# Optimization experiments

Measured on AMD Instinct MI355X. Metric: run time of the kernel, lower is better.

## Reference

```python
import jax, jax.numpy as jnp
import numpy as np

GRID_SIZE = 30
HIDDEN = 16

def _rbf_kan_layer(x, base_weight, spline_weight, grid):
    # x: [N, in], base_weight: [out, in], spline_weight: [in*G, out]
    base = x @ base_weight.T                                   # [N, out]
    basis = jnp.exp(-20.0 * (x[..., None] - grid) ** 2)        # [N, in, G]
    basis = basis.reshape(x.shape[0], -1)                      # [N, in*G]
    return base + basis @ spline_weight


def setup_inputs() -> dict:
    key = jax.random.key(0)
    ks = jax.random.split(key, 6)
    T = 100000
    t = (jnp.arange(T, dtype=jnp.float32) / T).reshape(T, 1)   # time grid in [0,1), dt = 1/T
    I_init = jax.random.uniform(ks[0], (1,), dtype=jnp.float32) * 0.1
    spline_weight1 = jax.random.normal(ks[1], (1 * GRID_SIZE, HIDDEN), dtype=jnp.float32) * 0.1
    base_weight1 = jax.random.normal(ks[2], (HIDDEN, 1), dtype=jnp.float32) * 0.1
    spline_weight2 = jax.random.normal(ks[3], (HIDDEN * GRID_SIZE, 1), dtype=jnp.float32) * 0.1
    base_weight2 = jax.random.normal(ks[4], (1, HIDDEN), dtype=jnp.float32) * 0.1
    gamma_param = jnp.array([2.0], dtype=jnp.float32)
    return {"t": t, "I_init": I_init,
            "spline_weight1": spline_weight1, "base_weight1": base_weight1,
            "spline_weight2": spline_weight2, "base_weight2": base_weight2,
            "gamma_param": gamma_param}


def reference(t, I_init, spline_weight1, base_weight1, spline_weight2, base_weight2, gamma_param):
    grid = jnp.linspace(0.0, 1.0, GRID_SIZE).astype(t.dtype)
    h = _rbf_kan_layer(t, base_weight1, spline_weight1, grid)      # [T, 16]
    out = _rbf_kan_layer(h, base_weight2, spline_weight2, grid)    # [T, 1]
    betas = jax.nn.softplus(out)                                   # [T, 1]
    gamma = jax.nn.softplus(gamma_param)                           # [1]
    dt = t[1, 0] - t[0, 0]

    I0 = I_init                                                    # [1]
    S0 = 1.0 - I0                                                  # [1]

    def step(carry, beta):
        S, I = carry
        dI = beta * S * I - gamma * I
        S_new = jnp.clip(S - beta * S * I * dt, 0.0, 1.0)
        I_new = jnp.clip(I + dI * dt, 0.0, 1.0)
        return (S_new, I_new), I_new

    _, sim_I = jax.lax.scan(step, (S0, I0), betas)                 # sim_I: [T, 1]
    return sim_I
```

## Files before the change

kernel.cpp:

```cpp
#include <hip/hip_runtime.h>
#include <hip/hip_bf16.h>

#define KAN_GRID 30
#define KAN_HID  16

#define PK   2500
#define PL   40
#define SNPT 10
#define CBLK ((PK + 255) / 256)

__global__ __launch_bounds__(256) void kan_betas_kernel(
    const float* __restrict__ t,
    const float* __restrict__ sw1,
    const float* __restrict__ bw1,
    const float* __restrict__ sw2,
    const float* __restrict__ bw2,
    float* __restrict__ beta_dt,
    int* __restrict__ bar,
    int T, int K, int L)
{
    __shared__ float s_sw1[KAN_GRID * KAN_HID];
    __shared__ float s_sw2[KAN_HID * KAN_GRID];
    __shared__ float s_bw1[KAN_HID];
    __shared__ float s_bw2[KAN_HID];

    if (bar && blockIdx.x == 0 && threadIdx.x < 2) bar[threadIdx.x] = 0;

    for (int i = threadIdx.x; i < KAN_GRID * KAN_HID; i += blockDim.x) {
        s_sw1[i] = sw1[i];
        s_sw2[i] = sw2[i];
    }
    if (threadIdx.x < KAN_HID) {
        s_bw1[threadIdx.x] = bw1[threadIdx.x];
        s_bw2[threadIdx.x] = bw2[threadIdx.x];
    }
    __syncthreads();

    int m = blockIdx.x * blockDim.x + threadIdx.x;
    if (m >= T) return;

    int n = (m % K) * L + m / K;

    float tv = t[n];
    float dt = t[1] - t[0];

    float h[KAN_HID];
#pragma unroll
    for (int j = 0; j < KAN_HID; ++j) h[j] = tv * s_bw1[j];

#pragma unroll
    for (int g = 0; g < KAN_GRID; ++g) {
        float d = tv - (float)g * (1.0f / 29.0f);
        float e = __expf(-20.0f * d * d);
#pragma unroll
        for (int j = 0; j < KAN_HID; ++j)
            h[j] = fmaf(e, s_sw1[g * KAN_HID + j], h[j]);
    }

    float out = 0.0f;
#pragma unroll
    for (int j = 0; j < KAN_HID; ++j) out = fmaf(h[j], s_bw2[j], out);

#pragma unroll
    for (int j = 0; j < KAN_HID; ++j) {
        float hv = h[j];
#pragma unroll
        for (int g = 0; g < KAN_GRID; ++g) {
            float d = hv - (float)g * (1.0f / 29.0f);
            out = fmaf(__expf(-20.0f * d * d), s_sw2[j * KAN_GRID + g], out);
        }
    }

    float beta = fmaxf(out, 0.0f) + log1pf(__expf(-fabsf(out)));
    beta_dt[m] = beta * dt;
}

#define STEP_O(BDT, DST)                            \
    {                                               \
        float x  = S * I;                           \
        float q  = fmaf(-gdt, I, I);                \
        float Sn = fmaf(-(BDT), x, S);              \
        float In = fmaf((BDT), x, q);               \
        Sn = fminf(fmaxf(Sn, 0.0f), 1.0f);          \
        In = fminf(fmaxf(In, 0.0f), 1.0f);          \
        S = Sn; I = In; (DST) = In;                 \
    }

#define STEP_J(BDT)                                          \
    {                                                        \
        float x  = S * I;                                    \
        float u  = (BDT) * I;                                \
        float v  = (BDT) * S;                                \
        float q  = fmaf(-gdt, I, I);                         \
        float Sn = fmaf(-(BDT), x, S);                       \
        float In = fmaf((BDT), x, q);                        \
        Sn = fminf(fmaxf(Sn, 0.0f), 1.0f);                   \
        In = fminf(fmaxf(In, 0.0f), 1.0f);                   \
        float w  = g1 + v;                                   \
        float a2 = fmaf(-v, jc, fmaf(-u, ja, ja));           \
        float b2 = fmaf(-v, jd, fmaf(-u, jb, jb));           \
        float c2 = fmaf(w, jc, u * ja);                      \
        float d2 = fmaf(w, jd, u * jb);                      \
        S = Sn; I = In; ja = a2; jb = b2; jc = c2; jd = d2;  \
    }

#define SOFTPLUS(X) (fmaxf((X), 0.0f) + log1pf(__expf(-fabsf(X))))

#define COMPOSE(ra,rb,rc,rd,rs,ri, La,Lb,Lc,Ld,Ls,Li, Ea,Eb,Ec,Ed,Es,Ei)   \
    {                                                                      \
        ra = fmaf(La, Ea, Lb * Ec);                                        \
        rb = fmaf(La, Eb, Lb * Ed);                                        \
        rc = fmaf(Lc, Ea, Ld * Ec);                                        \
        rd = fmaf(Lc, Eb, Ld * Ed);                                        \
        rs = fmaf(La, Es, fmaf(Lb, Ei, Ls));                               \
        ri = fmaf(Lc, Es, fmaf(Ld, Ei, Li));                               \
    }

__device__ __forceinline__ void grid_barrier(int* bar, int nblk) {
    __syncthreads();
    __threadfence();
    if (threadIdx.x == 0) {
        __hip_atomic_fetch_add(bar, 1, __ATOMIC_RELEASE,
                               __HIP_MEMORY_SCOPE_AGENT);
        while (__hip_atomic_load(bar, __ATOMIC_RELAXED,
                                 __HIP_MEMORY_SCOPE_AGENT) < nblk)
            __builtin_amdgcn_s_sleep(1);
    }
    __syncthreads();
    __threadfence();
}

__device__ __forceinline__ void block_affine_scan(
    const float* __restrict__ ja, const float* __restrict__ jb,
    const float* __restrict__ jc, const float* __restrict__ jd,
    const float* __restrict__ cs, const float* __restrict__ ci,
    int K, float S0, float I0,
    float2* g_lds, float (*wm)[6], float (*we)[6])
{
    int tid  = threadIdx.x;
    int lane = tid & 63;
    int wid  = tid >> 6;

    float Fa[SNPT], Fb[SNPT], Fc[SNPT], Fd[SNPT], Fs[SNPT], Fi[SNPT];
    float ma = 1.0f, mb = 0.0f, mc = 0.0f, md = 1.0f, ms = 0.0f, mi = 0.0f;
#pragma unroll
    for (int i = 0; i < SNPT; ++i) {
        int e = tid * SNPT + i;
        if (e < K) {
            Fa[i] = ja[e]; Fb[i] = jb[e]; Fc[i] = jc[e];
            Fd[i] = jd[e]; Fs[i] = cs[e]; Fi[i] = ci[e];
        } else {
            Fa[i] = 1.0f; Fb[i] = 0.0f; Fc[i] = 0.0f;
            Fd[i] = 1.0f; Fs[i] = 0.0f; Fi[i] = 0.0f;
        }
        float na, nb, nc, nd, ns, ni;
        COMPOSE(na,nb,nc,nd,ns,ni, Fa[i],Fb[i],Fc[i],Fd[i],Fs[i],Fi[i],
                                   ma,mb,mc,md,ms,mi);
        ma=na; mb=nb; mc=nc; md=nd; ms=ns; mi=ni;
    }

    for (int off = 1; off < 64; off <<= 1) {
        float pa = __shfl_up(ma, off), pb = __shfl_up(mb, off);
        float pc = __shfl_up(mc, off), pd = __shfl_up(md, off);
        float ps = __shfl_up(ms, off), pi = __shfl_up(mi, off);
        if (lane >= off) {
            float na, nb, nc, nd, ns, ni;
            COMPOSE(na,nb,nc,nd,ns,ni, ma,mb,mc,md,ms,mi, pa,pb,pc,pd,ps,pi);
            ma=na; mb=nb; mc=nc; md=nd; ms=ns; mi=ni;
        }
    }

    if (lane == 63) {
        wm[wid][0]=ma; wm[wid][1]=mb; wm[wid][2]=mc;
        wm[wid][3]=md; wm[wid][4]=ms; wm[wid][5]=mi;
    }
    __syncthreads();

    if (tid == 0) {
        float ra=1.0f, rb=0.0f, rc=0.0f, rd=1.0f, rs=0.0f, ri=0.0f;
        for (int w = 0; w < 4; ++w) {
            we[w][0]=ra; we[w][1]=rb; we[w][2]=rc;
            we[w][3]=rd; we[w][4]=rs; we[w][5]=ri;
            float na, nb, nc, nd, ns, ni;
            COMPOSE(na,nb,nc,nd,ns,ni,
                    wm[w][0],wm[w][1],wm[w][2],wm[w][3],wm[w][4],wm[w][5],
                    ra,rb,rc,rd,rs,ri);
            ra=na; rb=nb; rc=nc; rd=nd; rs=ns; ri=ni;
        }
    }
    __syncthreads();

    float xa = __shfl_up(ma, 1), xb = __shfl_up(mb, 1);
    float xc = __shfl_up(mc, 1), xd = __shfl_up(md, 1);
    float xs = __shfl_up(ms, 1), xi = __shfl_up(mi, 1);
    if (lane == 0) { xa=1.0f; xb=0.0f; xc=0.0f; xd=1.0f; xs=0.0f; xi=0.0f; }
    float Ca, Cb, Cc, Cd, Cs, Ci;
    COMPOSE(Ca,Cb,Cc,Cd,Cs,Ci, xa,xb,xc,xd,xs,xi,
            we[wid][0],we[wid][1],we[wid][2],we[wid][3],we[wid][4],we[wid][5]);

#pragma unroll
    for (int i = 0; i < SNPT; ++i) {
        int e = tid * SNPT + i;
        if (e < K) {
            float gS = fmaf(Ca, S0, fmaf(Cb, I0, Cs));
            float gI = fmaf(Cc, S0, fmaf(Cd, I0, Ci));
            g_lds[e] = make_float2(gS, gI);
        }
        float na, nb, nc, nd, ns, ni;
        COMPOSE(na,nb,nc,nd,ns,ni, Fa[i],Fb[i],Fc[i],Fd[i],Fs[i],Fi[i],
                                   Ca,Cb,Cc,Cd,Cs,Ci);
        Ca=na; Cb=nb; Cc=nc; Cd=nd; Cs=ns; Ci=ni;
    }
    __syncthreads();
}

template<int L>
__global__ __launch_bounds__(256, 1) void sir_fused_kernel(
    const float* __restrict__ t,
    const float* __restrict__ I_init,
    const float* __restrict__ gamma_param,
    const float* __restrict__ beta_t,
    float* __restrict__ A,
    float* __restrict__ B,
    int* __restrict__ bar,
    float* __restrict__ out,
    int K)
{
    __shared__ float2 g_lds[PK];
    __shared__ float wm[4][6], we[4][6];

    float dt = t[1] - t[0];
    float gdt = SOFTPLUS(gamma_param[0]) * dt;
    float g1 = 1.0f - gdt;
    float I0 = I_init[0];
    float S0 = 1.0f - I0;

    int k = blockIdx.x * blockDim.x + threadIdx.x;

    float b[L];
    if (k < K) {
#pragma unroll
        for (int s = 0; s < L; ++s) b[s] = beta_t[s * K + k];
    }

    if (k < K) {
        float S = S0, I = I0;
        float ja = 1.0f, jb = 0.0f, jc = 0.0f, jd = 1.0f;
#pragma unroll
        for (int s = 0; s < L; ++s) { float bdt = b[s]; STEP_J(bdt); }
        A[k]       = ja; A[K + k]   = jb; A[2*K + k] = jc; A[3*K + k] = jd;
        A[4*K + k] = S - fmaf(ja, S0, jb * I0);
        A[5*K + k] = I - fmaf(jc, S0, jd * I0);
    }
    grid_barrier(bar, gridDim.x);

    block_affine_scan(A, A + K, A + 2*K, A + 3*K, A + 4*K, A + 5*K,
                      K, S0, I0, g_lds, wm, we);
    if (k < K) {
        float2 g = g_lds[k];
        float S = g.x, I = g.y;
        float ja = 1.0f, jb = 0.0f, jc = 0.0f, jd = 1.0f;
#pragma unroll
        for (int s = 0; s < L; ++s) { float bdt = b[s]; STEP_J(bdt); }
        B[k]       = ja; B[K + k]   = jb; B[2*K + k] = jc; B[3*K + k] = jd;
        B[4*K + k] = S - fmaf(ja, g.x, jb * g.y);
        B[5*K + k] = I - fmaf(jc, g.x, jd * g.y);
    }
    grid_barrier(bar + 1, gridDim.x);

    block_affine_scan(B, B + K, B + 2*K, B + 3*K, B + 4*K, B + 5*K,
                      K, S0, I0, g_lds, wm, we);
    if (k < K) {
        float2 g = g_lds[k];
        float S = g.x, I = g.y;
        float4* o4 = (float4*)(out + (size_t)k * L);
#pragma unroll
        for (int i = 0; i < L / 4; ++i) {
            float4 r;
            STEP_O(b[4*i],     r.x);
            STEP_O(b[4*i + 1], r.y);
            STEP_O(b[4*i + 2], r.z);
            STEP_O(b[4*i + 3], r.w);
            o4[i] = r;
        }
    }
}

__global__ void kan_sir_scan_kernel(
    const float* __restrict__ t,
    const float* __restrict__ I_init,
    const float* __restrict__ gamma_param,
    const float* beta_dt,
    float* out,
    int T)
{
    if (threadIdx.x != 0 || blockIdx.x != 0) return;

    float dt = t[1] - t[0];
    float gdt = SOFTPLUS(gamma_param[0]) * dt;

    float I = I_init[0];
    float S = 1.0f - I;

    const float4* b4 = (const float4*)beta_dt;
    float4* o4 = (float4*)out;
    int nvec = T >> 2;

    const int PF = 8;
    float4 buf[PF];
#pragma unroll
    for (int i = 0; i < PF; ++i)
        buf[i] = (i < nvec) ? b4[i] : float4{0.0f, 0.0f, 0.0f, 0.0f};

    for (int base = 0; base < nvec; base += PF) {
#pragma unroll
        for (int i = 0; i < PF; ++i) {
            int c = base + i;
            if (c >= nvec) break;
            float4 b = buf[i];
            int nxt = c + PF;
            if (nxt < nvec) buf[i] = b4[nxt];

            float4 r;
            STEP_O(b.x, r.x);
            STEP_O(b.y, r.y);
            STEP_O(b.z, r.z);
            STEP_O(b.w, r.w);
            o4[c] = r;
        }
    }
    for (int n = nvec << 2; n < T; ++n) {
        float bdt = beta_dt[n];
        float r;
        STEP_O(bdt, r);
        out[n] = r;
    }
}

extern "C" void kernel_launch(void* const* d_in, const int* in_sizes, int n_in,
                              void* d_out, int out_size, void* d_ws, size_t ws_size,
                              hipStream_t stream) {
    const float* t      = (const float*)d_in[0];
    const float* I_init = (const float*)d_in[1];
    const float* sw1    = (const float*)d_in[2];
    const float* bw1    = (const float*)d_in[3];
    const float* sw2    = (const float*)d_in[4];
    const float* bw2    = (const float*)d_in[5];
    const float* gp     = (const float*)d_in[6];
    int T = in_sizes[0];

    float* outf = (float*)d_out;
    float* ws   = (float*)d_ws;
    int bblocks = (T + 255) / 256;

    const int K = PK;
    size_t need = ((size_t)T + 12 * K) * sizeof(float) + 2 * sizeof(int);
    bool fast = (T == PK * PL) && (ws_size >= need);

    if (fast) {
        float* beta_t = ws;
        float* A = ws + T;
        float* B = A + 6 * K;
        int* bar = (int*)(B + 6 * K);

        kan_betas_kernel<<<bblocks, 256, 0, stream>>>(t, sw1, bw1, sw2, bw2,
                                                      beta_t, bar, T, K, PL);
        sir_fused_kernel<PL><<<CBLK, 256, 0, stream>>>(
            t, I_init, gp, beta_t, A, B, bar, outf, K);
    } else {
        float* betab = (ws_size >= (size_t)T * sizeof(float)) ? ws : outf;
        kan_betas_kernel<<<bblocks, 256, 0, stream>>>(t, sw1, bw1, sw2, bw2,
                                                      betab, nullptr, T, T, 1);
        kan_sir_scan_kernel<<<1, 64, 0, stream>>>(t, I_init, gp, betab, outf, T);
    }
}
```

Before: 43.13 us.

## Fuse KAN beta evaluation and SIR scan into a single persistent mega-kernel

Merges the beta-evaluation kernel and the chunked SIR scan kernel into one launch. The first nbeta blocks compute betas and signal an atomic counter, and the last CBLK scan blocks spin on that counter before starting. The aim is to remove one kernel launch and the inter-kernel gap. In exchange it adds a hipMemsetAsync to reset the barriers, and it depends on the scan blocks becoming resident alongside the beta blocks, which risks deadlock or spin overhead if scheduling order is unfavourable. Shared-memory use per block also grows because the weight arrays and g_lds now share one kernel.

```diff
diff --git a/kernel.cpp b/kernel.cpp
--- a/kernel.cpp
+++ b/kernel.cpp
@@ -8,72 +8,6 @@
 #define PL   40
 #define SNPT 10
 #define CBLK ((PK + 255) / 256)
-
-__global__ __launch_bounds__(256) void kan_betas_kernel(
-    const float* __restrict__ t,
-    const float* __restrict__ sw1,
-    const float* __restrict__ bw1,
-    const float* __restrict__ sw2,
-    const float* __restrict__ bw2,
-    float* __restrict__ beta_dt,
-    int* __restrict__ bar,
-    int T, int K, int L)
-{
-    __shared__ float s_sw1[KAN_GRID * KAN_HID];
-    __shared__ float s_sw2[KAN_HID * KAN_GRID];
-    __shared__ float s_bw1[KAN_HID];
-    __shared__ float s_bw2[KAN_HID];
-
-    if (bar && blockIdx.x == 0 && threadIdx.x < 2) bar[threadIdx.x] = 0;
-
-    for (int i = threadIdx.x; i < KAN_GRID * KAN_HID; i += blockDim.x) {
-        s_sw1[i] = sw1[i];
-        s_sw2[i] = sw2[i];
-    }
-    if (threadIdx.x < KAN_HID) {
-        s_bw1[threadIdx.x] = bw1[threadIdx.x];
-        s_bw2[threadIdx.x] = bw2[threadIdx.x];
-    }
-    __syncthreads();
-
-    int m = blockIdx.x * blockDim.x + threadIdx.x;
-    if (m >= T) return;
-
-    int n = (m % K) * L + m / K;
-
-    float tv = t[n];
-    float dt = t[1] - t[0];
-
-    float h[KAN_HID];
-#pragma unroll
-    for (int j = 0; j < KAN_HID; ++j) h[j] = tv * s_bw1[j];
-
-#pragma unroll
-    for (int g = 0; g < KAN_GRID; ++g) {
-        float d = tv - (float)g * (1.0f / 29.0f);
-        float e = __expf(-20.0f * d * d);
-#pragma unroll
-        for (int j = 0; j < KAN_HID; ++j)
-            h[j] = fmaf(e, s_sw1[g * KAN_HID + j], h[j]);
-    }
-
-    float out = 0.0f;
-#pragma unroll
-    for (int j = 0; j < KAN_HID; ++j) out = fmaf(h[j], s_bw2[j], out);
-
-#pragma unroll
-    for (int j = 0; j < KAN_HID; ++j) {
-        float hv = h[j];
-#pragma unroll
-        for (int g = 0; g < KAN_GRID; ++g) {
-            float d = hv - (float)g * (1.0f / 29.0f);
-            out = fmaf(__expf(-20.0f * d * d), s_sw2[j * KAN_GRID + g], out);
-        }
-    }
-
-    float beta = fmaxf(out, 0.0f) + log1pf(__expf(-fabsf(out)));
-    beta_dt[m] = beta * dt;
-}
 
 #define STEP_O(BDT, DST)                            \
     {                                               \
@@ -116,6 +50,39 @@
         ri = fmaf(Lc, Es, fmaf(Ld, Ei, Li));                               \
     }
 
+__device__ __forceinline__ float kan_beta_eval(
+    float tv, const float* s_sw1, const float* s_sw2,
+    const float* s_bw1, const float* s_bw2, float dt)
+{
+    float h[KAN_HID];
+#pragma unroll
+    for (int j = 0; j < KAN_HID; ++j) h[j] = tv * s_bw1[j];
+
+#pragma unroll
+    for (int g = 0; g < KAN_GRID; ++g) {
+        float d = tv - (float)g * (1.0f / 29.0f);
+        float e = __expf(-20.0f * d * d);
+#pragma unroll
+        for (int j = 0; j < KAN_HID; ++j)
+            h[j] = fmaf(e, s_sw1[g * KAN_HID + j], h[j]);
+    }
+
+    float out = 0.0f;
+#pragma unroll
+    for (int j = 0; j < KAN_HID; ++j) out = fmaf(h[j], s_bw2[j], out);
+
+#pragma unroll
+    for (int j = 0; j < KAN_HID; ++j) {
+        float hv = h[j];
+#pragma unroll
+        for (int g = 0; g < KAN_GRID; ++g) {
+            float d = hv - (float)g * (1.0f / 29.0f);
+            out = fmaf(__expf(-20.0f * d * d), s_sw2[j * KAN_GRID + g], out);
+        }
+    }
+    return SOFTPLUS(out) * dt;
+}
+
 __device__ __forceinline__ void grid_barrier(int* bar, int nblk) {
     __syncthreads();
     __threadfence();
@@ -215,19 +182,63 @@
 }
 
 template<int L>
-__global__ __launch_bounds__(256, 1) void sir_fused_kernel(
+__global__ __launch_bounds__(256, 1) void kan_sir_mega_kernel(
     const float* __restrict__ t,
     const float* __restrict__ I_init,
     const float* __restrict__ gamma_param,
-    const float* __restrict__ beta_t,
+    const float* __restrict__ sw1,
+    const float* __restrict__ bw1,
+    const float* __restrict__ sw2,
+    const float* __restrict__ bw2,
+    float* __restrict__ beta_t,
     float* __restrict__ A,
     float* __restrict__ B,
     int* __restrict__ bar,
     float* __restrict__ out,
-    int K)
+    int T, int K, int nbeta)
 {
+    __shared__ float s_sw1[KAN_GRID * KAN_HID];
+    __shared__ float s_sw2[KAN_HID * KAN_GRID];
+    __shared__ float s_bw1[KAN_HID];
+    __shared__ float s_bw2[KAN_HID];
     __shared__ float2 g_lds[PK];
     __shared__ float wm[4][6], we[4][6];
+
+    int bid = blockIdx.x;
+    int tid = threadIdx.x;
+
+    if (bid < nbeta) {
+        for (int i = tid; i < KAN_GRID * KAN_HID; i += blockDim.x) {
+            s_sw1[i] = sw1[i];
+            s_sw2[i] = sw2[i];
+        }
+        if (tid < KAN_HID) {
+            s_bw1[tid] = bw1[tid];
+            s_bw2[tid] = bw2[tid];
+        }
+        __syncthreads();
+
+        int m = bid * 256 + tid;
+        if (m < T) {
+            int n = (m % K) * L + m / K;
+            float dt = t[1] - t[0];
+            beta_t[m] = kan_beta_eval(t[n], s_sw1, s_sw2, s_bw1, s_bw2, dt);
+        }
+        __syncthreads();
+        __threadfence();
+        if (tid == 0)
+            __hip_atomic_fetch_add(bar, 1, __ATOMIC_RELEASE,
+                                   __HIP_MEMORY_SCOPE_AGENT);
+        return;
+    }
+
+    if (tid == 0) {
+        while (__hip_atomic_load(bar, __ATOMIC_RELAXED,
+                                 __HIP_MEMORY_SCOPE_AGENT) < nbeta)
+            __builtin_amdgcn_s_sleep(1);
+    }
+    __syncthreads();
+    __threadfence();
 
     float dt = t[1] - t[0];
     float gdt = SOFTPLUS(gamma_param[0]) * dt;
@@ -235,7 +246,7 @@
     float I0 = I_init[0];
     float S0 = 1.0f - I0;
 
-    int k = blockIdx.x * blockDim.x + threadIdx.x;
+    int k = (bid - nbeta) * 256 + tid;
 
     float b[L];
     if (k < K) {
@@ -252,7 +263,7 @@
         A[4*K + k] = S - fmaf(ja, S0, jb * I0);
         A[5*K + k] = I - fmaf(jc, S0, jd * I0);
     }
-    grid_barrier(bar, gridDim.x);
+    grid_barrier(bar + 1, CBLK);
 
     block_affine_scan(A, A + K, A + 2*K, A + 3*K, A + 4*K, A + 5*K,
                       K, S0, I0, g_lds, wm, we);
@@ -266,7 +277,7 @@
         B[4*K + k] = S - fmaf(ja, g.x, jb * g.y);
         B[5*K + k] = I - fmaf(jc, g.x, jd * g.y);
     }
-    grid_barrier(bar + 1, gridDim.x);
+    grid_barrier(bar + 2, CBLK);
 
     block_affine_scan(B, B + K, B + 2*K, B + 3*K, B + 4*K, B + 5*K,
                       K, S0, I0, g_lds, wm, we);
@@ -284,6 +295,36 @@
             o4[i] = r;
         }
     }
+}
+
+__global__ __launch_bounds__(256) void kan_betas_kernel(
+    const float* __restrict__ t,
+    const float* __restrict__ sw1,
+    const float* __restrict__ bw1,
+    const float* __restrict__ sw2,
+    const float* __restrict__ bw2,
+    float* __restrict__ beta_dt,
+    int T)
+{
+    __shared__ float s_sw1[KAN_GRID * KAN_HID];
+    __shared__ float s_sw2[KAN_HID * KAN_GRID];
+    __shared__ float s_bw1[KAN_HID];
+    __shared__ float s_bw2[KAN_HID];
+
+    for (int i = threadIdx.x; i < KAN_GRID * KAN_HID; i += blockDim.x) {
+        s_sw1[i] = sw1[i];
+        s_sw2[i] = sw2[i];
+    }
+    if (threadIdx.x < KAN_HID) {
+        s_bw1[threadIdx.x] = bw1[threadIdx.x];
+        s_bw2[threadIdx.x] = bw2[threadIdx.x];
+    }
+    __syncthreads();
+
+    int m = blockIdx.x * blockDim.x + threadIdx.x;
+    if (m >= T) return;
+    float dt = t[1] - t[0];
+    beta_dt[m] = kan_beta_eval(t[m], s_sw1, s_sw2, s_bw1, s_bw2, dt);
 }
 
 __global__ void kan_sir_scan_kernel(
@@ -351,10 +392,10 @@
 
     float* outf = (float*)d_out;
     float* ws   = (float*)d_ws;
-    int bblocks = (T + 255) / 256;
+    int nbeta = (T + 255) / 256;
 
     const int K = PK;
-    size_t need = ((size_t)T + 12 * K) * sizeof(float) + 2 * sizeof(int);
+    size_t need = ((size_t)T + 12 * K) * sizeof(float) + 3 * sizeof(int);
     bool fast = (T == PK * PL) && (ws_size >= need);
 
     if (fast) {
@@ -363,14 +404,14 @@
         float* B = A + 6 * K;
         int* bar = (int*)(B + 6 * K);
 
-        kan_betas_kernel<<<bblocks, 256, 0, stream>>>(t, sw1, bw1, sw2, bw2,
-                                                      beta_t, bar, T, K, PL);
-        sir_fused_kernel<PL><<<CBLK, 256, 0, stream>>>(
-            t, I_init, gp, beta_t, A, B, bar, outf, K);
+        hipMemsetAsync(bar, 0, 3 * sizeof(int), stream);
+        kan_sir_mega_kernel<PL><<<nbeta + CBLK, 256, 0, stream>>>(
+            t, I_init, gp, sw1, bw1, sw2, bw2,
+            beta_t, A, B, bar, outf, T, K, nbeta);
     } else {
         float* betab = (ws_size >= (size_t)T * sizeof(float)) ? ws : outf;
-        kan_betas_kernel<<<bblocks, 256, 0, stream>>>(t, sw1, bw1, sw2, bw2,
-                                                      betab, nullptr, T, T, 1);
+        kan_betas_kernel<<<nbeta, 256, 0, stream>>>(t, sw1, bw1, sw2, bw2,
+                                                    betab, T);
         kan_sir_scan_kernel<<<1, 64, 0, stream>>>(t, I_init, gp, betab, outf, T);
     }
 }
```

New measurement: 74.16 us. 72.0% more time.
